# Kernel optimization log

Hardware: AMD Instinct MI355X
Metric: run time of the kernel (lower is better)

The kernel has to match this reference:

```python
import jax, jax.numpy as jnp
import numpy as np

B, S, D, H = 2, 2048, 512, 8
DK = D // H

def setup_inputs() -> dict:
    key = jax.random.key(0)
    ks = jax.random.split(key, 13)
    inp = {
        'query': jax.random.normal(ks[0], (B, S, D), jnp.float32),
        'key': jax.random.normal(ks[1], (B, S, D), jnp.float32),
        'value': jax.random.normal(ks[2], (B, S, D), jnp.float32),
        'group_prob': jax.random.uniform(ks[3], (B, S, S), jnp.float32),
        'mask': jax.random.randint(ks[4], (B, S, S), 0, 2, jnp.int32),
        'Wq': jax.random.normal(ks[5], (D, D), jnp.float32) * 0.02,
        'bq': jax.random.normal(ks[6], (D,), jnp.float32) * 0.02,
        'Wk': jax.random.normal(ks[7], (D, D), jnp.float32) * 0.02,
        'bk': jax.random.normal(ks[8], (D,), jnp.float32) * 0.02,
        'Wv': jax.random.normal(ks[9], (D, D), jnp.float32) * 0.02,
        'bv': jax.random.normal(ks[10], (D,), jnp.float32) * 0.02,
        'Wo': jax.random.normal(ks[11], (D, D), jnp.float32) * 0.02,
        'bo': jax.random.normal(ks[12], (D,), jnp.float32) * 0.02,
    }
    return inp

def reference(query, key, value, group_prob, mask, Wq, bq, Wk, bk, Wv, bv, Wo, bo):
    # project and split heads: [B,S,D] -> [B,H,S,dk]
    def proj(x, W, b):
        return (x @ W.T + b).reshape(B, S, H, DK).transpose(0, 2, 1, 3)
    q = proj(query, Wq, bq)
    k = proj(key, Wk, bk)
    v = proj(value, Wv, bv)
    scale = 1.0 / np.sqrt(DK).astype(np.float32)
    scores = jnp.einsum('bhqd,bhkd->bhqk', q, k) * scale  # [B,H,S,S]
    # allowed = mask | identity-diagonal; disallowed positions get -1e9
    diag = jnp.eye(S, dtype=bool)
    allowed = (mask.astype(bool) | diag)[:, None, :, :]  # [B,1,S,S]
    scores = jnp.where(allowed, scores, jnp.float32(-1e9))
    p_attn = jax.nn.softmax(scores, axis=-1) * group_prob[:, None, :, :]
    # dropout is identity in eval/deterministic mode
    x = jnp.einsum('bhqk,bhkd->bhqd', p_attn, v)  # [B,H,S,dk]
    x = x.transpose(0, 2, 1, 3).reshape(B, S, D)
    return x @ Wo.T + bo
```

## Files before the change

### kernel.cpp

```cpp
#include <hip/hip_runtime.h>
#include <hip/hip_bf16.h>
#include <cstdint>
#include <cstddef>

typedef __attribute__((ext_vector_type(8))) short bf16x8;
typedef __attribute__((ext_vector_type(4))) float f32x4;
typedef __attribute__((address_space(3))) void lds_void;
typedef const __attribute__((address_space(1))) void g_void;

constexpr int Bc = 2, Sc = 2048, Dc = 512, Hc = 8, DKc = 64;
constexpr int SPLIT = 2;
constexpr int NKT = Sc / 64;
constexpr int KT_PER = NKT / SPLIT;
constexpr float CSC = 0.18033688011112042f;

struct alignas(16) us8 { unsigned short u[8]; };
struct alignas(8) us4 { unsigned short u[4]; };

__device__ __forceinline__ unsigned short f2bf(float x) {
  union { float f; unsigned int u; } v; v.f = x;
  unsigned int r = (v.u + 0x7FFFu + ((v.u >> 16) & 1u)) >> 16;
  return (unsigned short)r;
}

__device__ __forceinline__ float bf2f(unsigned short u) {
  union { unsigned int u; float f; } v; v.u = ((unsigned int)u) << 16;
  return v.f;
}

__device__ __forceinline__ us8 cvt8(float4 a, float4 b) {
  us8 o;
  o.u[0] = f2bf(a.x); o.u[1] = f2bf(a.y); o.u[2] = f2bf(a.z); o.u[3] = f2bf(a.w);
  o.u[4] = f2bf(b.x); o.u[5] = f2bf(b.y); o.u[6] = f2bf(b.z); o.u[7] = f2bf(b.w);
  return o;
}

struct CArgs { const float* src[7]; unsigned short* dst[7]; int n8[7]; };

__global__ __launch_bounds__(256)
void cvt_multi(CArgs a)
{
  const int y = blockIdx.y;
  const float* s = a.src[y];
  unsigned short* d = a.dst[y];
  const int n8 = a.n8[y];
  int i = blockIdx.x * blockDim.x + threadIdx.x;
  const int stride = gridDim.x * blockDim.x;
  for (; i < n8; i += stride) {
    float4 va = ((const float4*)s)[(size_t)i * 2];
    float4 vb = ((const float4*)s)[(size_t)i * 2 + 1];
    ((us8*)d)[i] = cvt8(va, vb);
  }
}

__global__ __launch_bounds__(256)
void cvt_gpm(const float* __restrict__ g, const int* __restrict__ m,
             unsigned short* __restrict__ out)
{
  const int idx = blockIdx.x;
  const int b = idx >> 10, rest = idx & 1023, qt = rest >> 5, kt = rest & 31;
  const int tid = threadIdx.x;
  const int colb = tid & 15, hi = (tid >> 4) & 3, wid = tid >> 6;
  const int q = qt * 64 + wid * 16 + colb;
  const int k0 = kt * 64 + hi * 4;
  const float* grow = g + ((size_t)b * Sc + q) * Sc + k0;
  const int* mrow = m + ((size_t)b * Sc + q) * Sc + k0;
  unsigned short vals[16];
#pragma unroll
  for (int n = 0; n < 4; ++n) {
    float4 gv = *(const float4*)(grow + n * 16);
    int4 mv = *(const int4*)(mrow + n * 16);
    const int kb = k0 + n * 16;
    const float gg[4] = {gv.x, gv.y, gv.z, gv.w};
    const int mm[4] = {mv.x, mv.y, mv.z, mv.w};
#pragma unroll
    for (int rr = 0; rr < 4; ++rr) {
      const bool allowed = (mm[rr] != 0) || (kb + rr == q);
      vals[n * 4 + rr] = allowed ? (unsigned short)(f2bf(gg[rr]) | 1u) : (unsigned short)0;
    }
  }
  us8* o = (us8*)(out + (((size_t)idx * 256) + tid) * 16);
  o[0] = *(us8*)&vals[0];
  o[1] = *(us8*)&vals[8];
}

struct GArgs {
  const unsigned short* A[3];
  const unsigned short* W[3];
  const float* bias[3];
  void* C[3];
  int mode[3];
  float osc[3];
};

__global__ __launch_bounds__(256)
void gemm128(GArgs ga)
{
  __shared__ unsigned short As[128][64];
  __shared__ unsigned short Bs[128][64];

  constexpr int K = 512, N = 512;
  const int z = blockIdx.z;
  const unsigned short* Ap = ga.A[z];
  const unsigned short* Wp = ga.W[z];
  const float* bias = ga.bias[z];
  const int mode = ga.mode[z];
  const float osc = ga.osc[z];

  const int tid = threadIdx.x, lane = tid & 63, w = tid >> 6;
  const int m0 = blockIdx.x * 128, n0 = blockIdx.y * 128;
  const int wm = w >> 1, wn = w & 1;
  const int colb = lane & 15, hi = lane >> 4, rowb = hi * 4;
  const int swz = (colb & 7) << 4;

  f32x4 acc[4][4];
#pragma unroll
  for (int i = 0; i < 4; ++i)
#pragma unroll
    for (int j = 0; j < 4; ++j) acc[i][j] = (f32x4){0.f, 0.f, 0.f, 0.f};

  const int lrow8 = lane >> 3;
  const int cb = ((lane & 7) * 16) ^ (lrow8 << 4);

  for (int k0 = 0; k0 < K; k0 += 64) {
    if (k0) __syncthreads();
#pragma unroll
    for (int i = 0; i < 4; ++i) {
      const int obase = w * 1024 + i * 4096;
      const int row = w * 8 + i * 32 + lrow8;
      const unsigned short* asrc = Ap + (size_t)(m0 + row) * K + k0 + (cb >> 1);
      const unsigned short* bsrc = Wp + (size_t)(n0 + row) * K + k0 + (cb >> 1);
      __builtin_amdgcn_global_load_lds((g_void*)asrc, (lds_void*)((char*)&As[0][0] + obase), 16, 0, 0);
      __builtin_amdgcn_global_load_lds((g_void*)bsrc, (lds_void*)((char*)&Bs[0][0] + obase), 16, 0, 0);
    }
    asm volatile("s_waitcnt vmcnt(0)" ::: "memory");
    __syncthreads();

    char* ab = (char*)&As[0][0];
    char* bb = (char*)&Bs[0][0];
#pragma unroll
    for (int kk = 0; kk < 2; ++kk) {
      bf16x8 af[4], bfr[4];
#pragma unroll
      for (int mf = 0; mf < 4; ++mf) {
        const int ar = wm * 64 + mf * 16 + colb;
        af[mf] = *(const bf16x8*)(ab + ar * 128 + ((kk * 64 + hi * 16) ^ swz));
      }
#pragma unroll
      for (int nf = 0; nf < 4; ++nf) {
        const int br = wn * 64 + nf * 16 + colb;
        bfr[nf] = *(const bf16x8*)(bb + br * 128 + ((kk * 64 + hi * 16) ^ swz));
      }
      __builtin_amdgcn_s_setprio(1);
#pragma unroll
      for (int mf = 0; mf < 4; ++mf)
#pragma unroll
        for (int nf = 0; nf < 4; ++nf)
          acc[mf][nf] = __builtin_amdgcn_mfma_f32_16x16x32_bf16(af[mf], bfr[nf], acc[mf][nf], 0, 0, 0);
      __builtin_amdgcn_s_setprio(0);
    }
  }

#pragma unroll
  for (int nf = 0; nf < 4; ++nf) {
    const int gn = n0 + wn * 64 + nf * 16 + colb;
    const float bv = bias[gn];
    if (mode == 1) {
      unsigned short* Cp = (unsigned short*)ga.C[z];
#pragma unroll
      for (int mf = 0; mf < 4; ++mf) {
        const int gm = m0 + wm * 64 + mf * 16 + rowb;
        const int bb_ = gm >> 11, ss = gm & (Sc - 1);
        us4 vv;
#pragma unroll
        for (int rr = 0; rr < 4; ++rr) vv.u[rr] = f2bf(acc[mf][nf][rr] + bv);
        *(us4*)(Cp + ((size_t)bb_ * N + gn) * Sc + ss) = vv;
      }
    } else if (mode == 0) {
      unsigned short* Cp = (unsigned short*)ga.C[z];
#pragma unroll
      for (int mf = 0; mf < 4; ++mf)
#pragma unroll
        for (int rr = 0; rr < 4; ++rr) {
          const int gm = m0 + wm * 64 + mf * 16 + rowb + rr;
          Cp[(size_t)gm * N + gn] = f2bf((acc[mf][nf][rr] + bv) * osc);
        }
    } else {
      float* Cp = (float*)ga.C[z];
#pragma unroll
      for (int mf = 0; mf < 4; ++mf)
#pragma unroll
        for (int rr = 0; rr < 4; ++rr) {
          const int gm = m0 + wm * 64 + mf * 16 + rowb + rr;
          Cp[(size_t)gm * N + gn] = acc[mf][nf][rr] + bv;
        }
    }
  }
}

__global__ __launch_bounds__(256, 4)
void attn_split(const unsigned short* __restrict__ Qb,
                const unsigned short* __restrict__ Kb,
                const unsigned short* __restrict__ Vt,
                const unsigned short* __restrict__ Gp,
                float* __restrict__ Pacc,
                float* __restrict__ Pml)
{
  __shared__ unsigned short Ks[2][64][64];
  __shared__ unsigned short Vs[2][64][64];
  __shared__ unsigned short Ps[4][16][64];

  const int tid = threadIdx.x, lane = tid & 63, wid = tid >> 6;
  const int bh = blockIdx.x, b = bh >> 3, h = bh & 7;
  const int qt = blockIdx.y, q0 = qt * 64;
  const int sp = blockIdx.z;
  const int kt0 = sp * KT_PER;

  const int colb = lane & 15;
  const int hi = lane >> 4;
  const int rowb = hi * 4;
  const int c3s = (colb & 7) << 4;

  bf16x8 qf[2];
  {
    const unsigned short* qp = Qb + ((size_t)(b * Sc + q0 + wid * 16 + colb) * Dc + h * DKc + hi * 8);
    qf[0] = *(const bf16x8*)qp;
    qf[1] = *(const bf16x8*)(qp + 32);
  }

  f32x4 acc[4] = {{0,0,0,0},{0,0,0,0},{0,0,0,0},{0,0,0,0}};
  float mrun = -1e30f, lrun = 0.f;

  auto stageKV = [&](int bufI, int kt) {
    const int k0 = kt * 64;
#pragma unroll
    for (int i = 0; i < 2; ++i) {
      const int obase = wid * 1024 + i * 4096;
      const int row = (obase >> 7) + (lane >> 3);
      const int cb = ((lane & 7) * 16) ^ ((row & 7) << 4);
      const unsigned short* ksrc = Kb + (size_t)(b * Sc + k0 + row) * Dc + h * DKc + (cb >> 1);
      const unsigned short* vsrc = Vt + ((size_t)b * Dc + h * DKc + row) * Sc + k0 + (cb >> 1);
      __builtin_amdgcn_global_load_lds((g_void*)ksrc, (lds_void*)((char*)&Ks[bufI][0][0] + obase), 16, 0, 0);
      __builtin_amdgcn_global_load_lds((g_void*)vsrc, (lds_void*)((char*)&Vs[bufI][0][0] + obase), 16, 0, 0);
    }
  };

  const unsigned short* gtile = Gp + (((size_t)(b * 1024 + qt * 32)) * 256 + tid) * 16;
  us8 gcur0, gcur1;
  auto loadG = [&](int kt, us8& g0, us8& g1) {
    const us8* p = (const us8*)(gtile + (size_t)kt * 4096);
    g0 = p[0]; g1 = p[1];
  };

  stageKV(0, kt0);
  loadG(kt0, gcur0, gcur1);
  asm volatile("s_waitcnt vmcnt(0)" ::: "memory");
  __syncthreads();

  int buf = 0;
  char* psbase = (char*)&Ps[wid][0][0];

  for (int j = 0; j < KT_PER; ++j) {
    const int kt = kt0 + j;
    us8 gn0, gn1;
    if (j + 1 < KT_PER) {
      stageKV(buf ^ 1, kt + 1);
      loadG(kt + 1, gn0, gn1);
    }

    f32x4 sf[4] = {{0,0,0,0},{0,0,0,0},{0,0,0,0},{0,0,0,0}};
    char* ksb = (char*)&Ks[buf][0][0];
    __builtin_amdgcn_s_setprio(1);
#pragma unroll
    for (int kk = 0; kk < 2; ++kk) {
#pragma unroll
      for (int n = 0; n < 4; ++n) {
        const int krow = n * 16 + colb;
        bf16x8 kf = *(const bf16x8*)(ksb + krow * 128 + ((kk * 64 + hi * 16) ^ ((krow & 7) << 4)));
        sf[n] = __builtin_amdgcn_mfma_f32_16x16x32_bf16(kf, qf[kk], sf[n], 0, 0, 0);
      }
    }
    __builtin_amdgcn_s_setprio(0);

    float tm = sf[0][0];
#pragma unroll
    for (int n = 0; n < 4; ++n)
#pragma unroll
      for (int rr = 0; rr < 4; ++rr) tm = fmaxf(tm, sf[n][rr]);
    tm = fmaxf(tm, __shfl_xor(tm, 16));
    tm = fmaxf(tm, __shfl_xor(tm, 32));

    if (__any(tm > mrun + 8.f)) {
      const float mnew = fmaxf(mrun, tm);
      const float alpha = __builtin_amdgcn_exp2f(mrun - mnew);
      mrun = mnew;
#pragma unroll
      for (int n = 0; n < 4; ++n)
#pragma unroll
        for (int rr = 0; rr < 4; ++rr) acc[n][rr] *= alpha;
      lrun *= alpha;
    }

    float rsum = 0.f;
    unsigned int pw[8];
#pragma unroll
    for (int n = 0; n < 4; ++n) {
#pragma unroll
      for (int s2 = 0; s2 < 2; ++s2) {
        const int jv = n * 4 + s2 * 2;
        const unsigned short u0 = (jv < 8) ? gcur0.u[jv] : gcur1.u[jv - 8];
        const unsigned short u1 = (jv + 1 < 8) ? gcur0.u[jv + 1] : gcur1.u[jv + 1 - 8];
        const float p0 = __builtin_amdgcn_exp2f(sf[n][s2 * 2]     - mrun);
        const float p1 = __builtin_amdgcn_exp2f(sf[n][s2 * 2 + 1] - mrun);
        rsum = fmaf(p0, (float)(u0 & 1u), rsum);
        rsum = fmaf(p1, (float)(u1 & 1u), rsum);
        const float q0v = p0 * bf2f(u0), q1v = p1 * bf2f(u1);
        asm("v_cvt_pk_bf16_f32 %0, %1, %2" : "=v"(pw[n * 2 + s2]) : "v"(q0v), "v"(q1v));
      }
    }
    rsum += __shfl_xor(rsum, 16);
    rsum += __shfl_xor(rsum, 32);
    lrun += rsum;

#pragma unroll
    for (int n = 0; n < 4; ++n) {
      const unsigned long long w64 = ((unsigned long long)pw[n * 2 + 1] << 32) | pw[n * 2];
      *(unsigned long long*)(psbase + colb * 128 + ((n * 32 + hi * 8) ^ c3s)) = w64;
    }

    char* vsb = (char*)&Vs[buf][0][0];
    __builtin_amdgcn_s_setprio(1);
#pragma unroll
    for (int kk = 0; kk < 2; ++kk) {
      bf16x8 pf = *(const bf16x8*)(psbase + colb * 128 + ((kk * 64 + hi * 16) ^ c3s));
#pragma unroll
      for (int n = 0; n < 4; ++n) {
        const int vrow = n * 16 + colb;
        bf16x8 vf = *(const bf16x8*)(vsb + vrow * 128 + ((kk * 64 + hi * 16) ^ ((vrow & 7) << 4)));
        acc[n] = __builtin_amdgcn_mfma_f32_16x16x32_bf16(vf, pf, acc[n], 0, 0, 0);
      }
    }
    __builtin_amdgcn_s_setprio(0);

    asm volatile("s_waitcnt vmcnt(0)" ::: "memory");
    __syncthreads();
    buf ^= 1;
    if (j + 1 < KT_PER) { gcur0 = gn0; gcur1 = gn1; }
  }

  const size_t blin = ((size_t)bh * 32 + qt) * SPLIT + sp;
  float* pa = Pacc + blin * 4096;
#pragma unroll
  for (int n = 0; n < 4; ++n)
#pragma unroll
    for (int rr = 0; rr < 4; ++rr)
      pa[(size_t)(n * 16 + rowb + rr) * 64 + wid * 16 + colb] = acc[n][rr];
  if (hi == 0) {
    float* pm = Pml + blin * 128;
    pm[wid * 16 + colb] = mrun;
    pm[64 + wid * 16 + colb] = lrun;
  }
}

__global__ __launch_bounds__(256)
void attn_reduce(const float* __restrict__ Pacc, const float* __restrict__ Pml,
                 unsigned short* __restrict__ Xb)
{
  const int gidx = blockIdx.x;
  const int bh = gidx >> 5, qt = gidx & 31;
  const int b = bh >> 3, h = bh & 7;
  const int tid = threadIdx.x;
  const int qi = tid & 63;
  const int d0 = (tid >> 6) * 16;
  const size_t pb = (size_t)gidx * SPLIT;

  float m[SPLIT], l[SPLIT];
  float mstar = -3.0e38f;
#pragma unroll
  for (int s = 0; s < SPLIT; ++s) {
    m[s] = Pml[(pb + s) * 128 + qi];
    l[s] = Pml[(pb + s) * 128 + 64 + qi];
    mstar = fmaxf(mstar, m[s]);
  }
  float w[SPLIT], denom = 0.f;
#pragma unroll
  for (int s = 0; s < SPLIT; ++s) { w[s] = __builtin_amdgcn_exp2f(m[s] - mstar); denom += w[s] * l[s]; }
  const float inv = 1.0f / denom;

  unsigned short vals[16];
#pragma unroll
  for (int j = 0; j < 16; ++j) {
    float a = 0.f;
#pragma unroll
    for (int s = 0; s < SPLIT; ++s)
      a += w[s] * Pacc[(pb + s) * 4096 + (size_t)(d0 + j) * 64 + qi];
    vals[j] = f2bf(a * inv);
  }
  unsigned short* xp = Xb + ((size_t)(b * Sc) + qt * 64 + qi) * Dc + h * DKc + d0;
  *(us8*)xp = *(us8*)&vals[0];
  *(us8*)(xp + 8) = *(us8*)&vals[8];
}

extern "C" void kernel_launch(void* const* d_in, const int* in_sizes, int n_in,
                              void* d_out, int out_size, void* d_ws, size_t ws_size,
                              hipStream_t stream)
{
  const float* query = (const float*)d_in[0];
  const float* key_  = (const float*)d_in[1];
  const float* value = (const float*)d_in[2];
  const float* gprob = (const float*)d_in[3];
  const int*   mask  = (const int*)d_in[4];
  const float* Wq = (const float*)d_in[5];
  const float* bq = (const float*)d_in[6];
  const float* Wk = (const float*)d_in[7];
  const float* bk = (const float*)d_in[8];
  const float* Wv = (const float*)d_in[9];
  const float* bv = (const float*)d_in[10];
  const float* Wo = (const float*)d_in[11];
  const float* bo = (const float*)d_in[12];
  float* out = (float*)d_out;

  const size_t elems = (size_t)Bc * Sc * Dc;
  const size_t gelems = (size_t)Bc * Sc * Sc;
  const size_t welems = (size_t)Dc * Dc;

  char* base = (char*)d_ws;
  unsigned short* Qb = (unsigned short*)(base);
  unsigned short* Kb = Qb + elems;
  unsigned short* Vt = Kb + elems;
  unsigned short* Xb = Vt + elems;
  unsigned short* Gp = Xb + elems;
  char* shared_region = (char*)(Gp + gelems);
  unsigned short* Ain = (unsigned short*)shared_region;
  unsigned short* Bin = Ain + elems;
  unsigned short* Cin = Bin + elems;
  float* Pacc = (float*)shared_region;
  float* Pml  = Pacc + (size_t)(Bc * Hc) * 32 * SPLIT * 4096;
  unsigned short* Wqb = (unsigned short*)(shared_region + (18u << 20));
  unsigned short* Wkb = Wqb + welems;
  unsigned short* Wvb = Wkb + welems;
  unsigned short* Wob = Wvb + welems;

  CArgs ca;
  ca.src[0] = query; ca.dst[0] = Ain; ca.n8[0] = (int)(elems / 8);
  ca.src[1] = key_;  ca.dst[1] = Bin; ca.n8[1] = (int)(elems / 8);
  ca.src[2] = value; ca.dst[2] = Cin; ca.n8[2] = (int)(elems / 8);
  ca.src[3] = Wq;    ca.dst[3] = Wqb; ca.n8[3] = (int)(welems / 8);
  ca.src[4] = Wk;    ca.dst[4] = Wkb; ca.n8[4] = (int)(welems / 8);
  ca.src[5] = Wv;    ca.dst[5] = Wvb; ca.n8[5] = (int)(welems / 8);
  ca.src[6] = Wo;    ca.dst[6] = Wob; ca.n8[6] = (int)(welems / 8);
  hipLaunchKernelGGL(cvt_multi, dim3(128, 7), dim3(256), 0, stream, ca);
  hipLaunchKernelGGL(cvt_gpm, dim3(2048), dim3(256), 0, stream, gprob, mask, Gp);

  GArgs gq;
  gq.A[0] = Ain; gq.W[0] = Wqb; gq.bias[0] = bq; gq.C[0] = (void*)Qb; gq.mode[0] = 0; gq.osc[0] = CSC;
  gq.A[1] = Bin; gq.W[1] = Wkb; gq.bias[1] = bk; gq.C[1] = (void*)Kb; gq.mode[1] = 0; gq.osc[1] = 1.0f;
  gq.A[2] = Cin; gq.W[2] = Wvb; gq.bias[2] = bv; gq.C[2] = (void*)Vt; gq.mode[2] = 1; gq.osc[2] = 1.0f;
  hipLaunchKernelGGL(gemm128, dim3(32, 4, 3), dim3(256), 0, stream, gq);

  dim3 ga(Bc * Hc, Sc / 64, SPLIT);
  hipLaunchKernelGGL(attn_split, ga, dim3(256), 0, stream, Qb, Kb, Vt, Gp, Pacc, Pml);
  hipLaunchKernelGGL(attn_reduce, dim3(Bc * Hc * 32), dim3(256), 0, stream, Pacc, Pml, Xb);

  GArgs go;
  go.A[0] = Xb; go.W[0] = Wob; go.bias[0] = bo; go.C[0] = (void*)out; go.mode[0] = 2; go.osc[0] = 1.0f;
  go.A[1] = Xb; go.W[1] = Wob; go.bias[1] = bo; go.C[1] = (void*)out; go.mode[1] = 2; go.osc[1] = 1.0f;
  go.A[2] = Xb; go.W[2] = Wob; go.bias[2] = bo; go.C[2] = (void*)out; go.mode[2] = 2; go.osc[2] = 1.0f;
  hipLaunchKernelGGL(gemm128, dim3(32, 4, 1), dim3(256), 0, stream, go);
}
```

Baseline: 102.9 us.

## Fuse activation fp32->bf16 conversion into projection GEMM and merge prepass kernels

Removes the separate bf16 conversion pass over query/key/value by loading fp32 activations directly in the projection GEMM and converting them while staging into LDS. The group_prob/mask packing and the weight conversion are merged into a single prepass launch. The GEMM N-tile shrinks from 128 to 64, which doubles the grid to improve occupancy. The trade-off is synchronous register-path loads for the A operand instead of async global-to-LDS copies, plus reloading the A tile twice across N blocks.

```diff
diff --git a/kernel.cpp b/kernel.cpp
--- a/kernel.cpp
+++ b/kernel.cpp
@@ -35,57 +35,58 @@
   return o;
 }
 
-struct CArgs { const float* src[7]; unsigned short* dst[7]; int n8[7]; };
+struct PArgs {
+  const float* g; const int* m; unsigned short* gp;
+  const float* wsrc[4]; unsigned short* wdst[4];
+};
 
 __global__ __launch_bounds__(256)
-void cvt_multi(CArgs a)
+void prepass(PArgs pa)
 {
-  const int y = blockIdx.y;
-  const float* s = a.src[y];
-  unsigned short* d = a.dst[y];
-  const int n8 = a.n8[y];
-  int i = blockIdx.x * blockDim.x + threadIdx.x;
-  const int stride = gridDim.x * blockDim.x;
-  for (; i < n8; i += stride) {
-    float4 va = ((const float4*)s)[(size_t)i * 2];
-    float4 vb = ((const float4*)s)[(size_t)i * 2 + 1];
-    ((us8*)d)[i] = cvt8(va, vb);
-  }
-}
-
-__global__ __launch_bounds__(256)
-void cvt_gpm(const float* __restrict__ g, const int* __restrict__ m,
-             unsigned short* __restrict__ out)
-{
-  const int idx = blockIdx.x;
-  const int b = idx >> 10, rest = idx & 1023, qt = rest >> 5, kt = rest & 31;
+  const int bx = blockIdx.x;
   const int tid = threadIdx.x;
-  const int colb = tid & 15, hi = (tid >> 4) & 3, wid = tid >> 6;
-  const int q = qt * 64 + wid * 16 + colb;
-  const int k0 = kt * 64 + hi * 4;
-  const float* grow = g + ((size_t)b * Sc + q) * Sc + k0;
-  const int* mrow = m + ((size_t)b * Sc + q) * Sc + k0;
-  unsigned short vals[16];
-#pragma unroll
-  for (int n = 0; n < 4; ++n) {
-    float4 gv = *(const float4*)(grow + n * 16);
-    int4 mv = *(const int4*)(mrow + n * 16);
-    const int kb = k0 + n * 16;
-    const float gg[4] = {gv.x, gv.y, gv.z, gv.w};
-    const int mm[4] = {mv.x, mv.y, mv.z, mv.w};
-#pragma unroll
-    for (int rr = 0; rr < 4; ++rr) {
-      const bool allowed = (mm[rr] != 0) || (kb + rr == q);
-      vals[n * 4 + rr] = allowed ? (unsigned short)(f2bf(gg[rr]) | 1u) : (unsigned short)0;
-    }
-  }
-  us8* o = (us8*)(out + (((size_t)idx * 256) + tid) * 16);
-  o[0] = *(us8*)&vals[0];
-  o[1] = *(us8*)&vals[8];
+  if (bx < 2048) {
+    const int idx = bx;
+    const int b = idx >> 10, rest = idx & 1023, qt = rest >> 5, kt = rest & 31;
+    const int colb = tid & 15, hi = (tid >> 4) & 3, wid = tid >> 6;
+    const int q = qt * 64 + wid * 16 + colb;
+    const int k0 = kt * 64 + hi * 4;
+    const float* grow = pa.g + ((size_t)b * Sc + q) * Sc + k0;
+    const int* mrow = pa.m + ((size_t)b * Sc + q) * Sc + k0;
+    unsigned short vals[16];
+#pragma unroll
+    for (int n = 0; n < 4; ++n) {
+      float4 gv = *(const float4*)(grow + n * 16);
+      int4 mv = *(const int4*)(mrow + n * 16);
+      const int kb = k0 + n * 16;
+      const float gg[4] = {gv.x, gv.y, gv.z, gv.w};
+      const int mm[4] = {mv.x, mv.y, mv.z, mv.w};
+#pragma unroll
+      for (int rr = 0; rr < 4; ++rr) {
+        const bool allowed = (mm[rr] != 0) || (kb + rr == q);
+        vals[n * 4 + rr] = allowed ? (unsigned short)(f2bf(gg[rr]) | 1u) : (unsigned short)0;
+      }
+    }
+    us8* o = (us8*)(pa.gp + (((size_t)idx * 256) + tid) * 16);
+    o[0] = *(us8*)&vals[0];
+    o[1] = *(us8*)&vals[8];
+  } else {
+    const int r = bx - 2048;
+    const int wi = r >> 3, sub = r & 7;
+    const float* s = pa.wsrc[wi];
+    unsigned short* d = pa.wdst[wi];
+#pragma unroll
+    for (int t = 0; t < 16; ++t) {
+      const int i = sub * 4096 + t * 256 + tid;
+      float4 a = ((const float4*)s)[(size_t)i * 2];
+      float4 b = ((const float4*)s)[(size_t)i * 2 + 1];
+      ((us8*)d)[i] = cvt8(a, b);
+    }
+  }
 }
 
 struct GArgs {
-  const unsigned short* A[3];
+  const void* A[3];
   const unsigned short* W[3];
   const float* bias[3];
   void* C[3];
@@ -93,31 +94,31 @@
   float osc[3];
 };
 
+template<int A_FP32>
 __global__ __launch_bounds__(256)
-void gemm128(GArgs ga)
+void gemm_bn64(GArgs ga)
 {
   __shared__ unsigned short As[128][64];
-  __shared__ unsigned short Bs[128][64];
+  __shared__ unsigned short Bs[64][64];
 
   constexpr int K = 512, N = 512;
   const int z = blockIdx.z;
-  const unsigned short* Ap = ga.A[z];
   const unsigned short* Wp = ga.W[z];
   const float* bias = ga.bias[z];
   const int mode = ga.mode[z];
   const float osc = ga.osc[z];
 
   const int tid = threadIdx.x, lane = tid & 63, w = tid >> 6;
-  const int m0 = blockIdx.x * 128, n0 = blockIdx.y * 128;
+  const int m0 = blockIdx.x * 128, n0 = blockIdx.y * 64;
   const int wm = w >> 1, wn = w & 1;
   const int colb = lane & 15, hi = lane >> 4, rowb = hi * 4;
   const int swz = (colb & 7) << 4;
 
-  f32x4 acc[4][4];
+  f32x4 acc[4][2];
 #pragma unroll
   for (int i = 0; i < 4; ++i)
 #pragma unroll
-    for (int j = 0; j < 4; ++j) acc[i][j] = (f32x4){0.f, 0.f, 0.f, 0.f};
+    for (int j = 0; j < 2; ++j) acc[i][j] = (f32x4){0.f, 0.f, 0.f, 0.f};
 
   const int lrow8 = lane >> 3;
   const int cb = ((lane & 7) * 16) ^ (lrow8 << 4);
@@ -125,13 +126,31 @@
   for (int k0 = 0; k0 < K; k0 += 64) {
     if (k0) __syncthreads();
 #pragma unroll
-    for (int i = 0; i < 4; ++i) {
-      const int obase = w * 1024 + i * 4096;
-      const int row = w * 8 + i * 32 + lrow8;
-      const unsigned short* asrc = Ap + (size_t)(m0 + row) * K + k0 + (cb >> 1);
+    for (int i = 0; i < 2; ++i) {
+      const int u = w + i * 4;
+      const int row = u * 8 + lrow8;
       const unsigned short* bsrc = Wp + (size_t)(n0 + row) * K + k0 + (cb >> 1);
-      __builtin_amdgcn_global_load_lds((g_void*)asrc, (lds_void*)((char*)&As[0][0] + obase), 16, 0, 0);
-      __builtin_amdgcn_global_load_lds((g_void*)bsrc, (lds_void*)((char*)&Bs[0][0] + obase), 16, 0, 0);
+      __builtin_amdgcn_global_load_lds((g_void*)bsrc, (lds_void*)((char*)&Bs[0][0] + u * 1024), 16, 0, 0);
+    }
+    if (A_FP32) {
+      const float* Af = (const float*)ga.A[z];
+#pragma unroll
+      for (int i = 0; i < 4; ++i) {
+        const int u = w * 4 + i;
+        const int row = u * 8 + lrow8;
+        const float* src = Af + (size_t)(m0 + row) * K + k0 + (cb >> 1);
+        float4 v0 = *(const float4*)src, v1 = *(const float4*)(src + 4);
+        *(us8*)((char*)&As[0][0] + u * 1024 + lane * 16) = cvt8(v0, v1);
+      }
+    } else {
+      const unsigned short* Ab = (const unsigned short*)ga.A[z];
+#pragma unroll
+      for (int i = 0; i < 4; ++i) {
+        const int u = w * 4 + i;
+        const int row = u * 8 + lrow8;
+        const unsigned short* asrc = Ab + (size_t)(m0 + row) * K + k0 + (cb >> 1);
+        __builtin_amdgcn_global_load_lds((g_void*)asrc, (lds_void*)((char*)&As[0][0] + u * 1024), 16, 0, 0);
+      }
     }
     asm volatile("s_waitcnt vmcnt(0)" ::: "memory");
     __syncthreads();
@@ -140,30 +159,30 @@
     char* bb = (char*)&Bs[0][0];
 #pragma unroll
     for (int kk = 0; kk < 2; ++kk) {
-      bf16x8 af[4], bfr[4];
+      bf16x8 af[4], bfr[2];
 #pragma unroll
       for (int mf = 0; mf < 4; ++mf) {
         const int ar = wm * 64 + mf * 16 + colb;
         af[mf] = *(const bf16x8*)(ab + ar * 128 + ((kk * 64 + hi * 16) ^ swz));
       }
 #pragma unroll
-      for (int nf = 0; nf < 4; ++nf) {
-        const int br = wn * 64 + nf * 16 + colb;
+      for (int nf = 0; nf < 2; ++nf) {
+        const int br = wn * 32 + nf * 16 + colb;
         bfr[nf] = *(const bf16x8*)(bb + br * 128 + ((kk * 64 + hi * 16) ^ swz));
       }
       __builtin_amdgcn_s_setprio(1);
 #pragma unroll
       for (int mf = 0; mf < 4; ++mf)
 #pragma unroll
-        for (int nf = 0; nf < 4; ++nf)
+        for (int nf = 0; nf < 2; ++nf)
           acc[mf][nf] = __builtin_amdgcn_mfma_f32_16x16x32_bf16(af[mf], bfr[nf], acc[mf][nf], 0, 0, 0);
       __builtin_amdgcn_s_setprio(0);
     }
   }
 
 #pragma unroll
-  for (int nf = 0; nf < 4; ++nf) {
-    const int gn = n0 + wn * 64 + nf * 16 + colb;
+  for (int nf = 0; nf < 2; ++nf) {
+    const int gn = n0 + wn * 32 + nf * 16 + colb;
     const float bv = bias[gn];
     if (mode == 1) {
       unsigned short* Cp = (unsigned short*)ga.C[z];
@@ -430,41 +449,34 @@
   unsigned short* Vt = Kb + elems;
   unsigned short* Xb = Vt + elems;
   unsigned short* Gp = Xb + elems;
-  char* shared_region = (char*)(Gp + gelems);
-  unsigned short* Ain = (unsigned short*)shared_region;
-  unsigned short* Bin = Ain + elems;
-  unsigned short* Cin = Bin + elems;
-  float* Pacc = (float*)shared_region;
-  float* Pml  = Pacc + (size_t)(Bc * Hc) * 32 * SPLIT * 4096;
-  unsigned short* Wqb = (unsigned short*)(shared_region + (18u << 20));
+  unsigned short* Wqb = Gp + gelems;
   unsigned short* Wkb = Wqb + welems;
   unsigned short* Wvb = Wkb + welems;
   unsigned short* Wob = Wvb + welems;
-
-  CArgs ca;
-  ca.src[0] = query; ca.dst[0] = Ain; ca.n8[0] = (int)(elems / 8);
-  ca.src[1] = key_;  ca.dst[1] = Bin; ca.n8[1] = (int)(elems / 8);
-  ca.src[2] = value; ca.dst[2] = Cin; ca.n8[2] = (int)(elems / 8);
-  ca.src[3] = Wq;    ca.dst[3] = Wqb; ca.n8[3] = (int)(welems / 8);
-  ca.src[4] = Wk;    ca.dst[4] = Wkb; ca.n8[4] = (int)(welems / 8);
-  ca.src[5] = Wv;    ca.dst[5] = Wvb; ca.n8[5] = (int)(welems / 8);
-  ca.src[6] = Wo;    ca.dst[6] = Wob; ca.n8[6] = (int)(welems / 8);
-  hipLaunchKernelGGL(cvt_multi, dim3(128, 7), dim3(256), 0, stream, ca);
-  hipLaunchKernelGGL(cvt_gpm, dim3(2048), dim3(256), 0, stream, gprob, mask, Gp);
+  float* Pacc = (float*)(Wob + welems);
+  float* Pml  = Pacc + (size_t)(Bc * Hc) * 32 * SPLIT * 4096;
+
+  PArgs pa;
+  pa.g = gprob; pa.m = mask; pa.gp = Gp;
+  pa.wsrc[0] = Wq; pa.wdst[0] = Wqb;
+  pa.wsrc[1] = Wk; pa.wdst[1] = Wkb;
+  pa.wsrc[2] = Wv; pa.wdst[2] = Wvb;
+  pa.wsrc[3] = Wo; pa.wdst[3] = Wob;
+  hipLaunchKernelGGL(prepass, dim3(2080), dim3(256), 0, stream, pa);
 
   GArgs gq;
-  gq.A[0] = Ain; gq.W[0] = Wqb; gq.bias[0] = bq; gq.C[0] = (void*)Qb; gq.mode[0] = 0; gq.osc[0] = CSC;
-  gq.A[1] = Bin; gq.W[1] = Wkb; gq.bias[1] = bk; gq.C[1] = (void*)Kb; gq.mode[1] = 0; gq.osc[1] = 1.0f;
-  gq.A[2] = Cin; gq.W[2] = Wvb; gq.bias[2] = bv; gq.C[2] = (void*)Vt; gq.mode[2] = 1; gq.osc[2] = 1.0f;
-  hipLaunchKernelGGL(gemm128, dim3(32, 4, 3), dim3(256), 0, stream, gq);
+  gq.A[0] = (const void*)query; gq.W[0] = Wqb; gq.bias[0] = bq; gq.C[0] = (void*)Qb; gq.mode[0] = 0; gq.osc[0] = CSC;
+  gq.A[1] = (const void*)key_;  gq.W[1] = Wkb; gq.bias[1] = bk; gq.C[1] = (void*)Kb; gq.mode[1] = 0; gq.osc[1] = 1.0f;
+  gq.A[2] = (const void*)value; gq.W[2] = Wvb; gq.bias[2] = bv; gq.C[2] = (void*)Vt; gq.mode[2] = 1; gq.osc[2] = 1.0f;
+  hipLaunchKernelGGL((gemm_bn64<1>), dim3(32, 8, 3), dim3(256), 0, stream, gq);
 
   dim3 ga(Bc * Hc, Sc / 64, SPLIT);
   hipLaunchKernelGGL(attn_split, ga, dim3(256), 0, stream, Qb, Kb, Vt, Gp, Pacc, Pml);
   hipLaunchKernelGGL(attn_reduce, dim3(Bc * Hc * 32), dim3(256), 0, stream, Pacc, Pml, Xb);
 
   GArgs go;
-  go.A[0] = Xb; go.W[0] = Wob; go.bias[0] = bo; go.C[0] = (void*)out; go.mode[0] = 2; go.osc[0] = 1.0f;
-  go.A[1] = Xb; go.W[1] = Wob; go.bias[1] = bo; go.C[1] = (void*)out; go.mode[1] = 2; go.osc[1] = 1.0f;
-  go.A[2] = Xb; go.W[2] = Wob; go.bias[2] = bo; go.C[2] = (void*)out; go.mode[2] = 2; go.osc[2] = 1.0f;
-  hipLaunchKernelGGL(gemm128, dim3(32, 4, 1), dim3(256), 0, stream, go);
-}
+  go.A[0] = (const void*)Xb; go.W[0] = Wob; go.bias[0] = bo; go.C[0] = (void*)out; go.mode[0] = 2; go.osc[0] = 1.0f;
+  go.A[1] = go.A[0]; go.W[1] = go.W[0]; go.bias[1] = go.bias[0]; go.C[1] = go.C[0]; go.mode[1] = 2; go.osc[1] = 1.0f;
+  go.A[2] = go.A[0]; go.W[2] = go.W[0]; go.bias[2] = go.bias[0]; go.C[2] = go.C[0]; go.mode[2] = 2; go.osc[2] = 1.0f;
+  hipLaunchKernelGGL((gemm_bn64<0>), dim3(32, 8, 1), dim3(256), 0, stream, go);
+}
```

Result: no change. 101.3 us (-1.6%).
